# Performance work log

Measured on AMD Instinct MI355X. Metric: run time of the kernel, lower is better.

## Reference

```python
import jax, jax.numpy as jnp
import numpy as np

V, D, H, L = 50000, 50, 50, 100   # vocab, input_dim, hidden_dim, latent_dim
WIN = 5
B = 65536
MARGIN = 1.0


def setup_inputs() -> dict:
    key = jax.random.key(0)
    ks = jax.random.split(key, 12)
    emb = jax.random.normal(ks[0], (V, D), jnp.float32) * 0.1
    emb = emb.at[0].set(0.0)  # padding_idx=0
    W1 = jax.random.normal(ks[1], (2 * D, H), jnp.float32) * 0.1
    b1 = jnp.zeros((H,), jnp.float32)
    Wmu = jax.random.normal(ks[2], (H, L), jnp.float32) * 0.1
    bmu = jnp.zeros((L,), jnp.float32)
    Wls = jax.random.normal(ks[3], (H, 1), jnp.float32) * 0.1
    bls = jnp.zeros((1,), jnp.float32)
    type_means_tbl = jax.random.normal(ks[4], (V, L), jnp.float32) * 0.1
    type_logvars_tbl = jax.random.normal(ks[5], (V, 1), jnp.float32) * 0.1
    centers = jax.random.randint(ks[6], (B,), 1, V, jnp.int32)
    contexts = jax.random.randint(ks[7], (B, 2 * WIN), 1, V, jnp.int32)
    neg_contexts = jax.random.randint(ks[8], (B, 2 * WIN), 1, V, jnp.int32)
    return {"emb": emb, "W1": W1, "b1": b1, "Wmu": Wmu, "bmu": bmu,
            "Wls": Wls, "bls": bls, "type_means_tbl": type_means_tbl,
            "type_logvars_tbl": type_logvars_tbl, "centers": centers,
            "contexts": contexts, "neg_contexts": neg_contexts}


def _kl(idx, post_mu, post_logsigma, type_means_tbl, type_logvars_tbl):
    # idx: [N] int; post_mu: [N,L]; post_logsigma: [N,1]
    post_sigma = jnp.exp(post_logsigma)                      # [N,1]
    type_mean = type_means_tbl[idx]                          # [N,L]
    type_logvar = type_logvars_tbl[idx]                      # [N,1]
    type_var = jnp.exp(type_logvar)                          # [N,1]
    var_division = post_sigma / type_var                     # [N,1]
    diff = post_mu - type_mean                               # [N,L]
    diff_term = jnp.sum(diff * diff, axis=1, keepdims=True) / type_var  # [N,1]
    logvar_division = type_logvar - post_logsigma            # [N,1]
    return 0.5 * ((var_division + diff_term + logvar_division)[:, 0] - L)  # [N]


def reference(emb, W1, b1, Wmu, bmu, Wls, bls, type_means_tbl, type_logvars_tbl,
              centers, contexts, neg_contexts):
    Bn, C = contexts.shape                                   # C = 2*window
    e_ctx = emb[contexts]                                    # [B,C,D]
    e_cen = emb[centers]                                     # [B,D]
    # concat(context_embed, center_repeat) along feature dim -> [B,C,2D]
    cat = jnp.concatenate(
        [e_ctx, jnp.broadcast_to(e_cen[:, None, :], (Bn, C, D))], axis=-1)
    h = jax.nn.relu(jnp.einsum('bcf,fh->bch', cat, W1) + b1).sum(axis=1)  # [B,H]
    mu = h @ Wmu + bmu                                       # [B,L]
    logsigma = h @ Wls + bls                                 # [B,1]
    # repeat each row 2*window times (matches repeat(1,2w).view(-1,L))
    mus = jnp.repeat(mu, C, axis=0)                          # [B*C,L]
    logsigmas = jnp.repeat(logsigma, C, axis=0)              # [B*C,1]
    kl_ctx = _kl(contexts.reshape(-1), mus, logsigmas, type_means_tbl, type_logvars_tbl)
    kl_neg = _kl(neg_contexts.reshape(-1), mus, logsigmas, type_means_tbl, type_logvars_tbl)
    kl_cen = _kl(centers, mu, logsigma, type_means_tbl, type_logvars_tbl)
    hinge = jnp.maximum(kl_ctx - kl_neg + MARGIN, 0.0)
    loss = hinge.sum() + kl_cen.sum()
    return loss / Bn
```

## Files before the change

kernel.cpp:

```cpp
#include <hip/hip_runtime.h>

namespace {
constexpr int V    = 50000;
constexpr int D    = 50;
constexpr int H    = 50;
constexpr int LDIM = 100;
constexpr int C    = 10;
constexpr int B    = 65536;
constexpr int NTILES = B / 16;

constexpr size_t OFF_EMB  = 0;
constexpr size_t OFF_TM   = OFF_EMB + (size_t)V * 64 * 2;
constexpr size_t OFF_W1T  = OFF_TM + (size_t)V * 128;
constexpr size_t OFF_W1B  = OFF_W1T + 2 * 4 * 64 * 8 * 2;
constexpr size_t OFF_WMU  = OFF_W1B + 2 * 4 * 64 * 8 * 2;
constexpr size_t OFF_B1P  = OFF_WMU + 2 * 7 * 64 * 8 * 2;
constexpr size_t OFF_BMUP = OFF_B1P + 64 * 4;
constexpr size_t OFF_WLSP = OFF_BMUP + 128 * 4;
constexpr size_t OFF_TT   = OFF_WLSP + 64 * 4;
constexpr size_t OFF_MUF  = OFF_TT + (size_t)V * 16;
constexpr size_t OFF_MSL  = OFF_MUF + (size_t)NTILES * 4 * 64 * 8;
constexpr size_t OFF_PART = OFF_MSL + (size_t)B * 16;
constexpr size_t WS_NEED  = OFF_PART + (size_t)NTILES * 4;

typedef __attribute__((ext_vector_type(8))) short short8;
typedef __attribute__((ext_vector_type(4))) float f32x4;
typedef unsigned long long ull;

__device__ __forceinline__ unsigned short f2bf(float x) {
  unsigned u = __builtin_bit_cast(unsigned, x);
  unsigned r = (u + 0x7FFFu + ((u >> 16) & 1u)) >> 16;
  return (unsigned short)r;
}

__global__ __launch_bounds__(256) void bsg_prep(
    const float* __restrict__ emb, const float* __restrict__ tm,
    const float* __restrict__ tlv, const float* __restrict__ W1,
    const float* __restrict__ Wmu, const float* __restrict__ b1,
    const float* __restrict__ bmu, const float* __restrict__ Wls,
    unsigned short* __restrict__ embB, unsigned char* __restrict__ tmF8,
    float4* __restrict__ tt4, unsigned short* __restrict__ w1t,
    unsigned short* __restrict__ w1b, unsigned short* __restrict__ wmuB,
    float* __restrict__ b1p, float* __restrict__ bmup, float* __restrict__ wlsp) {
  const int EMB_T = V * 8;
  const int TM_T  = V * 8;
  const int stride = gridDim.x * blockDim.x;
  for (int t = blockIdx.x * blockDim.x + threadIdx.x; t < EMB_T + TM_T; t += stride) {
    if (t < EMB_T) {
      int v = t >> 3, c = t & 7, k0 = c * 8;
      unsigned short r[8];
#pragma unroll
      for (int e = 0; e < 8; ++e) {
        int k = k0 + e;
        r[e] = f2bf(k < D ? emb[(size_t)v * D + k] : 0.f);
      }
      uint4 o;
      o.x = (unsigned)r[0] | ((unsigned)r[1] << 16);
      o.y = (unsigned)r[2] | ((unsigned)r[3] << 16);
      o.z = (unsigned)r[4] | ((unsigned)r[5] << 16);
      o.w = (unsigned)r[6] | ((unsigned)r[7] << 16);
      ((uint4*)(embB + (size_t)v * 64))[c] = o;
    } else {
      int t2 = t - EMB_T;
      int v = t2 >> 3, c = t2 & 7, k0 = c * 16;
      float val[16];
#pragma unroll
      for (int e = 0; e < 16; ++e) {
        int k = k0 + e;
        val[e] = (k < LDIM) ? tm[(size_t)v * LDIM + k] : 0.f;
      }
      uint4 o;
      unsigned dw[4];
      float sq = 0.f;
#pragma unroll
      for (int j = 0; j < 4; ++j) {
        int d = __builtin_amdgcn_cvt_pk_fp8_f32(val[4 * j + 0], val[4 * j + 1], 0, false);
        d = __builtin_amdgcn_cvt_pk_fp8_f32(val[4 * j + 2], val[4 * j + 3], d, true);
        dw[j] = (unsigned)d;
        float q0 = __builtin_amdgcn_cvt_f32_fp8(d, 0);
        float q1 = __builtin_amdgcn_cvt_f32_fp8(d, 1);
        float q2 = __builtin_amdgcn_cvt_f32_fp8(d, 2);
        float q3 = __builtin_amdgcn_cvt_f32_fp8(d, 3);
        sq = fmaf(q0, q0, sq); sq = fmaf(q1, q1, sq);
        sq = fmaf(q2, q2, sq); sq = fmaf(q3, q3, sq);
      }
      o.x = dw[0]; o.y = dw[1]; o.z = dw[2]; o.w = dw[3];
      ((uint4*)(tmF8 + (size_t)v * 128))[c] = o;
#pragma unroll
      for (int off = 1; off < 8; off <<= 1) sq += __shfl_xor(sq, off);
      if (c == 0) {
        float tl = tlv[v];
        float4 q;
        q.x = tl; q.y = __expf(-tl); q.z = sq; q.w = 0.f;
        tt4[v] = q;
      }
    }
  }
  if (blockIdx.x == 0) {
    const int tid = threadIdx.x;
    for (int id = tid; id < 1024; id += 256) {
      int half = id >> 9, rem = id & 511;
      int ks = rem >> 8, nt = (rem >> 6) & 3, l = rem & 63;
      unsigned short r[8];
      int n = nt * 16 + (l & 15);
#pragma unroll
      for (int e = 0; e < 8; ++e) {
        int f = ks * 32 + ((l >> 4) << 3) + e;
        float v = (f < D && n < H) ? W1[(size_t)(half * D + f) * H + n] : 0.f;
        r[e] = f2bf(v);
      }
      uint4 o;
      o.x = (unsigned)r[0] | ((unsigned)r[1] << 16);
      o.y = (unsigned)r[2] | ((unsigned)r[3] << 16);
      o.z = (unsigned)r[4] | ((unsigned)r[5] << 16);
      o.w = (unsigned)r[6] | ((unsigned)r[7] << 16);
      unsigned short* dst = half ? w1b : w1t;
      ((uint4*)dst)[(ks * 4 + nt) * 64 + l] = o;
    }
    for (int id = tid; id < 896; id += 256) {
      int ks = id / 448, rem = id % 448;
      int nt = rem >> 6, l = rem & 63;
      unsigned short r[8];
      int n = nt * 16 + (l & 15);
#pragma unroll
      for (int e = 0; e < 8; ++e) {
        int j = ks * 32 + ((l >> 4) << 3) + e;
        float v = (j < H && n < LDIM) ? Wmu[(size_t)j * LDIM + n] : 0.f;
        r[e] = f2bf(v);
      }
      uint4 o;
      o.x = (unsigned)r[0] | ((unsigned)r[1] << 16);
      o.y = (unsigned)r[2] | ((unsigned)r[3] << 16);
      o.z = (unsigned)r[4] | ((unsigned)r[5] << 16);
      o.w = (unsigned)r[6] | ((unsigned)r[7] << 16);
      ((uint4*)wmuB)[(ks * 7 + nt) * 64 + l] = o;
    }
    if (tid < 64)  b1p[tid]  = (tid < H)    ? b1[tid]  : 0.f;
    if (tid < 128) bmup[tid] = (tid < LDIM) ? bmu[tid] : 0.f;
    if (tid < 64)  wlsp[tid] = (tid < H)    ? Wls[tid] : 0.f;
  }
}

__global__ __launch_bounds__(256, 3) void bsg_mlp(
    const unsigned short* __restrict__ embB,
    const unsigned short* __restrict__ w1t,
    const unsigned short* __restrict__ w1b,
    const unsigned short* __restrict__ wmuB,
    const float* __restrict__ b1p, const float* __restrict__ bmup,
    const float* __restrict__ wlsp, const float* __restrict__ bls,
    const int* __restrict__ centers, const int* __restrict__ contexts,
    ull* __restrict__ muF, float4* __restrict__ msl) {
  __shared__ unsigned short hlds[32][64];
  __shared__ unsigned char kb[2][16][128];
  __shared__ float logsp[2][32];
  __shared__ float musq_p[2][2][16];
  __shared__ char stg[4][4 * 2048];

  const int tid = threadIdx.x;
  const int w = tid >> 6, l = tid & 63;
  const int srow = l & 15, kc = l >> 4;
  const int st = w & 1, np = w >> 1;
  const int sblk = blockIdx.x * 32;
  const int sg = sblk + st * 16 + srow;
  const int s3 = srow & 3;

  char* kbbase = (char*)&kb[0][0][0];
  auto kb_ptr = [&](int st_, int s_, int kbyte) -> char* {
    return kbbase + st_ * 2048 + s_ * 128 + (kbyte ^ ((s_ & 7) << 4));
  };

  {
    int st_ = tid >> 7, rem = tid & 127;
    int s_ = rem >> 3, j = rem & 7;
    *(unsigned short*)kb_ptr(st_, s_, 112 + 2 * j) = 0;
  }

  char* myl = &stg[w][0];
  const int cofs = ((kc ^ s3) << 4);
  const int aoff = ((kc ^ s3) << 8) + (srow << 4);

  int rid[11];
  rid[0] = centers[sg];
#pragma unroll
  for (int c = 0; c < 10; ++c) rid[1 + c] = contexts[sg * 10 + c];

  const short8* w1tF = (const short8*)w1t;
  const short8* w1bF = (const short8*)w1b;

  short8 Bz[2][2], Bt[2][2];
#pragma unroll
  for (int n2 = 0; n2 < 2; ++n2)
#pragma unroll
    for (int ks = 0; ks < 2; ++ks) {
      Bz[n2][ks] = w1bF[(ks * 4 + 2 * np + n2) * 64 + l];
      Bt[n2][ks] = w1tF[(ks * 4 + 2 * np + n2) * 64 + l];
    }
  float b1v[2] = {b1p[(2 * np + 0) * 16 + srow], b1p[(2 * np + 1) * 16 + srow]};

  const unsigned char* embBy = (const unsigned char*)embB;

  f32x4 Z0 = {0.f, 0.f, 0.f, 0.f}, Z1 = {0.f, 0.f, 0.f, 0.f};
  f32x4 hv0 = {0.f, 0.f, 0.f, 0.f}, hv1 = {0.f, 0.f, 0.f, 0.f};

#define MLP_STAGE(T)                                                         \
  do {                                                                       \
    const unsigned char* src_ = embBy + (size_t)rid[(T)] * 128 + cofs;       \
    char* d0_ = myl + ((T) & 3) * 2048;                                      \
    __builtin_amdgcn_global_load_lds(                                        \
        (const __attribute__((address_space(1))) unsigned int*)src_,         \
        (__attribute__((address_space(3))) unsigned int*)d0_, 16, 0, 0);     \
    __builtin_amdgcn_global_load_lds(                                        \
        (const __attribute__((address_space(1))) unsigned int*)(src_ + 64),  \
        (__attribute__((address_space(3))) unsigned int*)(d0_ + 1024),       \
        16, 0, 0);                                                           \
  } while (0)

#define MLP_STEP(T, NW)                                                      \
  do {                                                                       \
    if ((T) + 3 < 11) MLP_STAGE((T) + 3);                                    \
    asm volatile("s_waitcnt vmcnt(" #NW ")" ::: "memory");                   \
    __builtin_amdgcn_sched_barrier(0);                                       \
    const char* sb_ = myl + ((T) & 3) * 2048;                                \
    short8 A0_ = *(const short8*)(sb_ + aoff);                               \
    short8 A1_ = *(const short8*)(sb_ + 1024 + aoff);                        \
    if ((T) == 0) {                                                          \
      Z0 = __builtin_amdgcn_mfma_f32_16x16x32_bf16(A0_, Bz[0][0], Z0, 0, 0, 0); \
      Z0 = __builtin_amdgcn_mfma_f32_16x16x32_bf16(A1_, Bz[0][1], Z0, 0, 0, 0); \
      Z1 = __builtin_amdgcn_mfma_f32_16x16x32_bf16(A0_, Bz[1][0], Z1, 0, 0, 0); \
      Z1 = __builtin_amdgcn_mfma_f32_16x16x32_bf16(A1_, Bz[1][1], Z1, 0, 0, 0); \
    } else {                                                                 \
      f32x4 ac0_ = {0.f, 0.f, 0.f, 0.f}, ac1_ = {0.f, 0.f, 0.f, 0.f};        \
      ac0_ = __builtin_amdgcn_mfma_f32_16x16x32_bf16(A0_, Bt[0][0], ac0_, 0, 0, 0); \
      ac0_ = __builtin_amdgcn_mfma_f32_16x16x32_bf16(A1_, Bt[0][1], ac0_, 0, 0, 0); \
      ac1_ = __builtin_amdgcn_mfma_f32_16x16x32_bf16(A0_, Bt[1][0], ac1_, 0, 0, 0); \
      ac1_ = __builtin_amdgcn_mfma_f32_16x16x32_bf16(A1_, Bt[1][1], ac1_, 0, 0, 0); \
      _Pragma("unroll")                                                      \
      for (int q = 0; q < 4; ++q) {                                          \
        hv0[q] += fmaxf(ac0_[q] + Z0[q] + b1v[0], 0.f);                      \
        hv1[q] += fmaxf(ac1_[q] + Z1[q] + b1v[1], 0.f);                      \
      }                                                                      \
    }                                                                        \
  } while (0)

  MLP_STAGE(0);
  MLP_STAGE(1);
  MLP_STAGE(2);

  MLP_STEP(0, 6); MLP_STEP(1, 6); MLP_STEP(2, 6); MLP_STEP(3, 6);
  MLP_STEP(4, 6); MLP_STEP(5, 6); MLP_STEP(6, 6); MLP_STEP(7, 6);
  MLP_STEP(8, 4); MLP_STEP(9, 2); MLP_STEP(10, 0);

#undef MLP_STEP
#undef MLP_STAGE

  {
    float wl0 = wlsp[(2 * np + 0) * 16 + srow];
    float wl1 = wlsp[(2 * np + 1) * 16 + srow];
    float lp[4];
#pragma unroll
    for (int q = 0; q < 4; ++q) lp[q] = hv0[q] * wl0 + hv1[q] * wl1;
#pragma unroll
    for (int off = 1; off < 16; off <<= 1)
#pragma unroll
      for (int q = 0; q < 4; ++q) lp[q] += __shfl_xor(lp[q], off);
    if (srow == 0) {
#pragma unroll
      for (int q = 0; q < 4; ++q) logsp[np][st * 16 + kc * 4 + q] = lp[q];
    }
  }
#pragma unroll
  for (int q = 0; q < 4; ++q) {
    hlds[st * 16 + kc * 4 + q][(2 * np + 0) * 16 + srow] = f2bf(hv0[q]);
    hlds[st * 16 + kc * 4 + q][(2 * np + 1) * 16 + srow] = f2bf(hv1[q]);
  }
  __syncthreads();

  {
    const short8* hrow = (const short8*)&hlds[st * 16 + srow][0];
    short8 Ah0 = hrow[kc], Ah1 = hrow[4 + kc];
    const short8* wmF = (const short8*)wmuB;
    f32x4 sqv = {0.f, 0.f, 0.f, 0.f};
    for (int nt = np; nt < 7; nt += 2) {
      short8 B0 = wmF[(0 * 7 + nt) * 64 + l];
      short8 B1 = wmF[(1 * 7 + nt) * 64 + l];
      f32x4 m = {0.f, 0.f, 0.f, 0.f};
      m = __builtin_amdgcn_mfma_f32_16x16x32_bf16(Ah0, B0, m, 0, 0, 0);
      m = __builtin_amdgcn_mfma_f32_16x16x32_bf16(Ah1, B1, m, 0, 0, 0);
      int lcol = nt * 16 + srow;
      float bm = bmup[lcol];
      float mv0 = m[0] + bm, mv1 = m[1] + bm, mv2 = m[2] + bm, mv3 = m[3] + bm;
      int d01 = __builtin_amdgcn_cvt_pk_fp8_f32(mv0, mv1, 0, false);
      int d23 = __builtin_amdgcn_cvt_pk_fp8_f32(mv2, mv3, 0, false);
      float q0 = __builtin_amdgcn_cvt_f32_fp8(d01, 0);
      float q1 = __builtin_amdgcn_cvt_f32_fp8(d01, 1);
      float q2 = __builtin_amdgcn_cvt_f32_fp8(d23, 0);
      float q3 = __builtin_amdgcn_cvt_f32_fp8(d23, 1);
      sqv[0] = fmaf(q0, q0, sqv[0]);
      sqv[1] = fmaf(q1, q1, sqv[1]);
      sqv[2] = fmaf(q2, q2, sqv[2]);
      sqv[3] = fmaf(q3, q3, sqv[3]);
      *(unsigned char*)kb_ptr(st, kc * 4 + 0, lcol) = (unsigned char)(d01 & 0xFF);
      *(unsigned char*)kb_ptr(st, kc * 4 + 1, lcol) = (unsigned char)((d01 >> 8) & 0xFF);
      *(unsigned char*)kb_ptr(st, kc * 4 + 2, lcol) = (unsigned char)(d23 & 0xFF);
      *(unsigned char*)kb_ptr(st, kc * 4 + 3, lcol) = (unsigned char)((d23 >> 8) & 0xFF);
    }
#pragma unroll
    for (int off = 1; off < 16; off <<= 1)
#pragma unroll
      for (int q = 0; q < 4; ++q) sqv[q] += __shfl_xor(sqv[q], off);
    if (srow == 0) {
#pragma unroll
      for (int q = 0; q < 4; ++q) musq_p[np][st][kc * 4 + q] = sqv[q];
    }
  }
  __syncthreads();

  if (w < 2) {
    size_t gt = (size_t)blockIdx.x * 2 + w;
#pragma unroll
    for (int ks = 0; ks < 4; ++ks) {
      ull v = *(const ull*)kb_ptr(w, srow, ks * 32 + kc * 8);
      muF[(gt * 4 + ks) * 64 + l] = v;
    }
  } else if (w == 2 && l < 32) {
    int s_ = l;
    float lg = bls[0] + logsp[0][s_] + logsp[1][s_];
    float msq = musq_p[0][s_ >> 4][s_ & 15] + musq_p[1][s_ >> 4][s_ & 15];
    float4 o;
    o.x = lg; o.y = __expf(lg); o.z = msq; o.w = 0.f;
    msl[sblk + s_] = o;
  }
}

__global__ __launch_bounds__(256) void bsg_kl(
    const unsigned char* __restrict__ tmF8, const float4* __restrict__ tt4,
    const ull* __restrict__ muF, const float4* __restrict__ msl,
    const int* __restrict__ centers, const int* __restrict__ contexts,
    const int* __restrict__ negctx, float* __restrict__ partials) {
  __shared__ char klds[4][4 * 2048];

  const int w = threadIdx.x >> 6, l = threadIdx.x & 63;
  const int gt = blockIdx.x * 4 + w;
  const int srow = l & 15, kc = l >> 4;
  const int s = gt * 16 + srow;
  const int s3 = srow & 3;

  char* myl = &klds[w][0];
  const int cofs = ((kc ^ s3) << 4);
  const int rA = ((((kc >> 1) ^ s3) * 16 + srow) * 16) + (kc & 1) * 8;
  const int rB = ((((2 + (kc >> 1)) ^ s3) * 16 + srow) * 16) + (kc & 1) * 8;

  ull Bmu[4];
#pragma unroll
  for (int ks = 0; ks < 4; ++ks) Bmu[ks] = muF[((size_t)gt * 4 + ks) * 64 + l];

  const float4 m = msl[s];
  const float lg = m.x, ps = m.y, msq = m.z;
  const bool isdiag = (kc == (srow >> 2));
  const int qd = srow & 3;

  int idx[21];
  idx[0] = centers[s];
#pragma unroll
  for (int c = 0; c < 10; ++c) idx[1 + c] = contexts[s * 10 + c];
#pragma unroll
  for (int c = 0; c < 10; ++c) idx[11 + c] = negctx[s * 10 + c];

  constexpr int ord[21] = {0, 1, 11, 2, 12, 3, 13, 4, 14, 5, 15,
                           6, 16, 7, 17, 8, 18, 9, 19, 10, 20};

  float4 ttb[4];
  float loss = 0.f, klc = 0.f;

#define KL_STAGE(T)                                                          \
  do {                                                                       \
    const unsigned char* src_ = tmF8 + (size_t)idx[ord[(T)]] * 128 + cofs;   \
    char* d0_ = myl + ((T) & 3) * 2048;                                      \
    __builtin_amdgcn_global_load_lds(                                        \
        (const __attribute__((address_space(1))) unsigned int*)src_,         \
        (__attribute__((address_space(3))) unsigned int*)d0_, 16, 0, 0);     \
    __builtin_amdgcn_global_load_lds(                                        \
        (const __attribute__((address_space(1))) unsigned int*)(src_ + 64),  \
        (__attribute__((address_space(3))) unsigned int*)(d0_ + 1024),       \
        16, 0, 0);                                                           \
    ttb[(T) & 3] = tt4[idx[ord[(T)]]];                                       \
  } while (0)

#define KL_STEP(T, NW)                                                       \
  do {                                                                       \
    if ((T) + 3 < 21) KL_STAGE((T) + 3);                                     \
    asm volatile("s_waitcnt vmcnt(" #NW ")" ::: "memory");                   \
    __builtin_amdgcn_sched_barrier(0);                                       \
    const char* kb_ = myl + ((T) & 3) * 2048;                                \
    ull a0_ = *(const ull*)(kb_ + rA);                                       \
    ull a1_ = *(const ull*)(kb_ + rB);                                       \
    ull a2_ = *(const ull*)(kb_ + rA + 1024);                                \
    ull a3_ = *(const ull*)(kb_ + rB + 1024);                                \
    f32x4 acc_ = {0.f, 0.f, 0.f, 0.f};                                       \
    acc_ = __builtin_amdgcn_mfma_f32_16x16x32_fp8_fp8((long)a0_, (long)Bmu[0], acc_, 0, 0, 0); \
    acc_ = __builtin_amdgcn_mfma_f32_16x16x32_fp8_fp8((long)a1_, (long)Bmu[1], acc_, 0, 0, 0); \
    acc_ = __builtin_amdgcn_mfma_f32_16x16x32_fp8_fp8((long)a2_, (long)Bmu[2], acc_, 0, 0, 0); \
    acc_ = __builtin_amdgcn_mfma_f32_16x16x32_fp8_fp8((long)a3_, (long)Bmu[3], acc_, 0, 0, 0); \
    float4 tv_ = ttb[(T) & 3];                                               \
    float dot_ = (qd & 2) ? ((qd & 1) ? acc_[3] : acc_[2])                   \
                          : ((qd & 1) ? acc_[1] : acc_[0]);                  \
    float dsum_ = msq + tv_.z - 2.f * dot_;                                  \
    float kl_ = 0.5f * (fmaf(ps + dsum_, tv_.y, tv_.x - lg) - (float)LDIM);  \
    if ((T) == 0)      loss += isdiag ? kl_ : 0.f;                           \
    else if ((T) & 1)  klc = kl_;                                            \
    else               loss += isdiag ? fmaxf(klc - kl_ + 1.f, 0.f) : 0.f;   \
  } while (0)

  KL_STAGE(0);
  KL_STAGE(1);
  KL_STAGE(2);

  KL_STEP(0, 6);  KL_STEP(1, 6);  KL_STEP(2, 6);  KL_STEP(3, 6);
  KL_STEP(4, 6);  KL_STEP(5, 6);  KL_STEP(6, 6);  KL_STEP(7, 6);
  KL_STEP(8, 6);  KL_STEP(9, 6);  KL_STEP(10, 6); KL_STEP(11, 6);
  KL_STEP(12, 6); KL_STEP(13, 6); KL_STEP(14, 6); KL_STEP(15, 6);
  KL_STEP(16, 6); KL_STEP(17, 6); KL_STEP(18, 4); KL_STEP(19, 2);
  KL_STEP(20, 0);

#undef KL_STEP
#undef KL_STAGE

#pragma unroll
  for (int off = 32; off > 0; off >>= 1) loss += __shfl_down(loss, off);
  if (l == 0) partials[gt] = loss;
}

__global__ __launch_bounds__(256) void bsg_reduce(const float* __restrict__ partials,
                                                  int n, float* __restrict__ out) {
  double v = 0.0;
  for (int i = threadIdx.x; i < n; i += 256) v += (double)partials[i];
#pragma unroll
  for (int off = 32; off > 0; off >>= 1) v += __shfl_down(v, off);
  __shared__ double ws4[4];
  if ((threadIdx.x & 63) == 0) ws4[threadIdx.x >> 6] = v;
  __syncthreads();
  if (threadIdx.x == 0) {
    double t = 0.0;
#pragma unroll
    for (int k = 0; k < 4; ++k) t += ws4[k];
    out[0] = (float)(t / (double)B);
  }
}

__device__ __forceinline__ float kl_term_fb(const float* mu, float ps, float logs,
                                            int idx, const float* tm_tbl,
                                            const float* tlv_tbl) {
  const float* tm = tm_tbl + (size_t)idx * LDIM;
  float tlv = tlv_tbl[idx];
  float d0 = 0.f, d1 = 0.f, d2 = 0.f, d3 = 0.f;
#pragma unroll
  for (int l = 0; l < LDIM; l += 4) {
    float4 t = *reinterpret_cast<const float4*>(tm + l);
    float a0 = mu[l] - t.x, a1 = mu[l + 1] - t.y;
    float a2 = mu[l + 2] - t.z, a3 = mu[l + 3] - t.w;
    d0 = fmaf(a0, a0, d0); d1 = fmaf(a1, a1, d1);
    d2 = fmaf(a2, a2, d2); d3 = fmaf(a3, a3, d3);
  }
  return 0.5f * (fmaf(ps + (d0 + d1) + (d2 + d3), __expf(-tlv), tlv - logs) - (float)LDIM);
}

__global__ __launch_bounds__(256) void bsg_fb(
    const float* __restrict__ emb, const float* __restrict__ W1,
    const float* __restrict__ b1, const float* __restrict__ Wmu,
    const float* __restrict__ bmu, const float* __restrict__ Wls,
    const float* __restrict__ bls, const float* __restrict__ tm_tbl,
    const float* __restrict__ tlv_tbl, const int* __restrict__ centers,
    const int* __restrict__ contexts, const int* __restrict__ negctx,
    float* __restrict__ partials) {
  const int b = blockIdx.x * 256 + threadIdx.x;
  const int cen = centers[b];
  float ecen[D];
  const float* ep = emb + (size_t)cen * D;
#pragma unroll
  for (int f = 0; f < D; f += 2) {
    float2 v = *reinterpret_cast<const float2*>(ep + f);
    ecen[f] = v.x; ecen[f + 1] = v.y;
  }
  float z[H];
#pragma unroll
  for (int j = 0; j < H; ++j) z[j] = b1[j];
#pragma unroll
  for (int f = 0; f < D; ++f) {
    float vf = ecen[f];
#pragma unroll
    for (int j = 0; j < H; ++j) z[j] = fmaf(vf, W1[(D + f) * H + j], z[j]);
  }
  float h[H];
#pragma unroll
  for (int j = 0; j < H; ++j) h[j] = 0.f;
  for (int c = 0; c < C; ++c) {
    const float* ecp = emb + (size_t)contexts[b * C + c] * D;
    float s[H];
#pragma unroll
    for (int j = 0; j < H; ++j) s[j] = z[j];
#pragma unroll
    for (int f = 0; f < D; ++f) {
      float vf = ecp[f];
#pragma unroll
      for (int j = 0; j < H; ++j) s[j] = fmaf(vf, W1[f * H + j], s[j]);
    }
#pragma unroll
    for (int j = 0; j < H; ++j) h[j] += fmaxf(s[j], 0.f);
  }
  float mu[LDIM];
#pragma unroll
  for (int l = 0; l < LDIM; ++l) mu[l] = bmu[l];
#pragma unroll
  for (int j = 0; j < H; ++j) {
    float hj = h[j];
#pragma unroll
    for (int l = 0; l < LDIM; ++l) mu[l] = fmaf(hj, Wmu[j * LDIM + l], mu[l]);
  }
  float logs = bls[0];
#pragma unroll
  for (int j = 0; j < H; ++j) logs = fmaf(h[j], Wls[j], logs);
  float ps = __expf(logs);
  float acc = kl_term_fb(mu, ps, logs, cen, tm_tbl, tlv_tbl);
  for (int c = 0; c < C; ++c) {
    float kc = kl_term_fb(mu, ps, logs, contexts[b * C + c], tm_tbl, tlv_tbl);
    float kn = kl_term_fb(mu, ps, logs, negctx[b * C + c], tm_tbl, tlv_tbl);
    acc += fmaxf(kc - kn + 1.f, 0.f);
  }
  float vs = acc;
#pragma unroll
  for (int off = 32; off > 0; off >>= 1) vs += __shfl_down(vs, off);
  __shared__ float wsum[4];
  if ((threadIdx.x & 63) == 0) wsum[threadIdx.x >> 6] = vs;
  __syncthreads();
  if (threadIdx.x == 0) {
    float t = 0.f;
#pragma unroll
    for (int k = 0; k < 4; ++k) t += wsum[k];
    partials[blockIdx.x] = t;
  }
}
}

extern "C" void kernel_launch(void* const* d_in, const int* in_sizes, int n_in,
                              void* d_out, int out_size, void* d_ws, size_t ws_size,
                              hipStream_t stream) {
  const float* emb     = (const float*)d_in[0];
  const float* W1      = (const float*)d_in[1];
  const float* b1      = (const float*)d_in[2];
  const float* Wmu     = (const float*)d_in[3];
  const float* bmu     = (const float*)d_in[4];
  const float* Wls     = (const float*)d_in[5];
  const float* bls     = (const float*)d_in[6];
  const float* tm      = (const float*)d_in[7];
  const float* tlv     = (const float*)d_in[8];
  const int*   centers = (const int*)d_in[9];
  const int*   ctx     = (const int*)d_in[10];
  const int*   negc    = (const int*)d_in[11];
  float* out = (float*)d_out;

  if (ws_size < WS_NEED + 1024) {
    float* partials = (float*)d_ws;
    bsg_fb<<<256, 256, 0, stream>>>(emb, W1, b1, Wmu, bmu, Wls, bls, tm, tlv,
                                    centers, ctx, negc, partials);
    bsg_reduce<<<1, 256, 0, stream>>>(partials, 256, out);
    return;
  }

  char* ws = (char*)d_ws;
  unsigned short* embB = (unsigned short*)(ws + OFF_EMB);
  unsigned char*  tmF8 = (unsigned char*)(ws + OFF_TM);
  unsigned short* w1t  = (unsigned short*)(ws + OFF_W1T);
  unsigned short* w1b  = (unsigned short*)(ws + OFF_W1B);
  unsigned short* wmuB = (unsigned short*)(ws + OFF_WMU);
  float* b1p  = (float*)(ws + OFF_B1P);
  float* bmup = (float*)(ws + OFF_BMUP);
  float* wlsp = (float*)(ws + OFF_WLSP);
  float4* tt4 = (float4*)(ws + OFF_TT);
  ull* muF    = (ull*)(ws + OFF_MUF);
  float4* msl = (float4*)(ws + OFF_MSL);
  float* partials = (float*)(ws + OFF_PART);

  bsg_prep<<<1024, 256, 0, stream>>>(emb, tm, tlv, W1, Wmu, b1, bmu, Wls,
                                     embB, tmF8, tt4, w1t, w1b, wmuB, b1p, bmup, wlsp);
  bsg_mlp<<<B / 32, 256, 0, stream>>>(embB, w1t, w1b, wmuB, b1p, bmup, wlsp, bls,
                                      centers, ctx, muF, msl);
  bsg_kl<<<NTILES / 4, 256, 0, stream>>>(tmF8, tt4, muF, msl, centers, ctx, negc,
                                         partials);
  bsg_reduce<<<1, 256, 0, stream>>>(partials, NTILES, out);
}
```

Baseline: 76.27 us.

## Fuse MLP and KL kernels, splitting context pairs across waves

Result: no change. 76.43 us (+0.2%).

```diff
diff --git a/kernel.cpp b/kernel.cpp
--- a/kernel.cpp
+++ b/kernel.cpp
@@ -7,7 +7,7 @@
 constexpr int LDIM = 100;
 constexpr int C    = 10;
 constexpr int B    = 65536;
-constexpr int NTILES = B / 16;
+constexpr int NPART = (B / 32) * 4;
 
 constexpr size_t OFF_EMB  = 0;
 constexpr size_t OFF_TM   = OFF_EMB + (size_t)V * 64 * 2;
@@ -18,10 +18,8 @@
 constexpr size_t OFF_BMUP = OFF_B1P + 64 * 4;
 constexpr size_t OFF_WLSP = OFF_BMUP + 128 * 4;
 constexpr size_t OFF_TT   = OFF_WLSP + 64 * 4;
-constexpr size_t OFF_MUF  = OFF_TT + (size_t)V * 16;
-constexpr size_t OFF_MSL  = OFF_MUF + (size_t)NTILES * 4 * 64 * 8;
-constexpr size_t OFF_PART = OFF_MSL + (size_t)B * 16;
-constexpr size_t WS_NEED  = OFF_PART + (size_t)NTILES * 4;
+constexpr size_t OFF_PART = OFF_TT + (size_t)V * 16;
+constexpr size_t WS_NEED  = OFF_PART + (size_t)NPART * 4;
 
 typedef __attribute__((ext_vector_type(8))) short short8;
 typedef __attribute__((ext_vector_type(4))) float f32x4;
@@ -141,15 +139,16 @@
   }
 }
 
-__global__ __launch_bounds__(256, 3) void bsg_mlp(
+__global__ __launch_bounds__(256, 3) void bsg_main(
     const unsigned short* __restrict__ embB,
+    const unsigned char* __restrict__ tmF8, const float4* __restrict__ tt4,
     const unsigned short* __restrict__ w1t,
     const unsigned short* __restrict__ w1b,
     const unsigned short* __restrict__ wmuB,
     const float* __restrict__ b1p, const float* __restrict__ bmup,
     const float* __restrict__ wlsp, const float* __restrict__ bls,
     const int* __restrict__ centers, const int* __restrict__ contexts,
-    ull* __restrict__ muF, float4* __restrict__ msl) {
+    const int* __restrict__ negctx, float* __restrict__ partials) {
   __shared__ unsigned short hlds[32][64];
   __shared__ unsigned char kb[2][16][128];
   __shared__ float logsp[2][32];
@@ -178,6 +177,8 @@
   char* myl = &stg[w][0];
   const int cofs = ((kc ^ s3) << 4);
   const int aoff = ((kc ^ s3) << 8) + (srow << 4);
+  const int rA = ((((kc >> 1) ^ s3) * 16 + srow) * 16) + (kc & 1) * 8;
+  const int rB = ((((2 + (kc >> 1)) ^ s3) * 16 + srow) * 16) + (kc & 1) * 8;
 
   int rid[11];
   rid[0] = centers[sg];
@@ -315,66 +316,33 @@
   }
   __syncthreads();
 
-  if (w < 2) {
-    size_t gt = (size_t)blockIdx.x * 2 + w;
-#pragma unroll
-    for (int ks = 0; ks < 4; ++ks) {
-      ull v = *(const ull*)kb_ptr(w, srow, ks * 32 + kc * 8);
-      muF[(gt * 4 + ks) * 64 + l] = v;
-    }
-  } else if (w == 2 && l < 32) {
-    int s_ = l;
-    float lg = bls[0] + logsp[0][s_] + logsp[1][s_];
-    float msq = musq_p[0][s_ >> 4][s_ & 15] + musq_p[1][s_ >> 4][s_ & 15];
-    float4 o;
-    o.x = lg; o.y = __expf(lg); o.z = msq; o.w = 0.f;
-    msl[sblk + s_] = o;
-  }
-}
-
-__global__ __launch_bounds__(256) void bsg_kl(
-    const unsigned char* __restrict__ tmF8, const float4* __restrict__ tt4,
-    const ull* __restrict__ muF, const float4* __restrict__ msl,
-    const int* __restrict__ centers, const int* __restrict__ contexts,
-    const int* __restrict__ negctx, float* __restrict__ partials) {
-  __shared__ char klds[4][4 * 2048];
-
-  const int w = threadIdx.x >> 6, l = threadIdx.x & 63;
-  const int gt = blockIdx.x * 4 + w;
-  const int srow = l & 15, kc = l >> 4;
-  const int s = gt * 16 + srow;
-  const int s3 = srow & 3;
-
-  char* myl = &klds[w][0];
-  const int cofs = ((kc ^ s3) << 4);
-  const int rA = ((((kc >> 1) ^ s3) * 16 + srow) * 16) + (kc & 1) * 8;
-  const int rB = ((((2 + (kc >> 1)) ^ s3) * 16 + srow) * 16) + (kc & 1) * 8;
-
-  ull Bmu[4];
-#pragma unroll
-  for (int ks = 0; ks < 4; ++ks) Bmu[ks] = muF[((size_t)gt * 4 + ks) * 64 + l];
-
-  const float4 m = msl[s];
-  const float lg = m.x, ps = m.y, msq = m.z;
+  const int p = np;
+  const float lg = bls[0] + logsp[0][st * 16 + srow] + logsp[1][st * 16 + srow];
+  const float ps = __expf(lg);
+  const float msq = musq_p[0][st][srow] + musq_p[1][st][srow];
   const bool isdiag = (kc == (srow >> 2));
   const int qd = srow & 3;
 
-  int idx[21];
-  idx[0] = centers[s];
-#pragma unroll
-  for (int c = 0; c < 10; ++c) idx[1 + c] = contexts[s * 10 + c];
-#pragma unroll
-  for (int c = 0; c < 10; ++c) idx[11 + c] = negctx[s * 10 + c];
-
-  constexpr int ord[21] = {0, 1, 11, 2, 12, 3, 13, 4, 14, 5, 15,
-                           6, 16, 7, 17, 8, 18, 9, 19, 10, 20};
+  ull Bmu[4];
+#pragma unroll
+  for (int ks = 0; ks < 4; ++ks)
+    Bmu[ks] = *(const ull*)kb_ptr(st, srow, ks * 32 + kc * 8);
+
+  int kidx[11];
+  kidx[0] = rid[0];
+#pragma unroll
+  for (int i = 0; i < 5; ++i) {
+    int c = p + 2 * i;
+    kidx[1 + 2 * i] = rid[1 + c];
+    kidx[2 + 2 * i] = negctx[sg * 10 + c];
+  }
 
   float4 ttb[4];
   float loss = 0.f, klc = 0.f;
 
 #define KL_STAGE(T)                                                          \
   do {                                                                       \
-    const unsigned char* src_ = tmF8 + (size_t)idx[ord[(T)]] * 128 + cofs;   \
+    const unsigned char* src_ = tmF8 + (size_t)kidx[(T)] * 128 + cofs;       \
     char* d0_ = myl + ((T) & 3) * 2048;                                      \
     __builtin_amdgcn_global_load_lds(                                        \
         (const __attribute__((address_space(1))) unsigned int*)src_,         \
@@ -383,12 +351,12 @@
         (const __attribute__((address_space(1))) unsigned int*)(src_ + 64),  \
         (__attribute__((address_space(3))) unsigned int*)(d0_ + 1024),       \
         16, 0, 0);                                                           \
-    ttb[(T) & 3] = tt4[idx[ord[(T)]]];                                       \
+    ttb[(T) & 3] = tt4[kidx[(T)]];                                           \
   } while (0)
 
 #define KL_STEP(T, NW)                                                       \
   do {                                                                       \
-    if ((T) + 3 < 21) KL_STAGE((T) + 3);                                     \
+    if ((T) + 3 < 11) KL_STAGE((T) + 3);                                     \
     asm volatile("s_waitcnt vmcnt(" #NW ")" ::: "memory");                   \
     __builtin_amdgcn_sched_barrier(0);                                       \
     const char* kb_ = myl + ((T) & 3) * 2048;                                \
@@ -406,7 +374,7 @@
                           : ((qd & 1) ? acc_[1] : acc_[0]);                  \
     float dsum_ = msq + tv_.z - 2.f * dot_;                                  \
     float kl_ = 0.5f * (fmaf(ps + dsum_, tv_.y, tv_.x - lg) - (float)LDIM);  \
-    if ((T) == 0)      loss += isdiag ? kl_ : 0.f;                           \
+    if ((T) == 0)      loss += (isdiag && p == 0) ? kl_ : 0.f;               \
     else if ((T) & 1)  klc = kl_;                                            \
     else               loss += isdiag ? fmaxf(klc - kl_ + 1.f, 0.f) : 0.f;   \
   } while (0)
@@ -415,19 +383,16 @@
   KL_STAGE(1);
   KL_STAGE(2);
 
-  KL_STEP(0, 6);  KL_STEP(1, 6);  KL_STEP(2, 6);  KL_STEP(3, 6);
-  KL_STEP(4, 6);  KL_STEP(5, 6);  KL_STEP(6, 6);  KL_STEP(7, 6);
-  KL_STEP(8, 6);  KL_STEP(9, 6);  KL_STEP(10, 6); KL_STEP(11, 6);
-  KL_STEP(12, 6); KL_STEP(13, 6); KL_STEP(14, 6); KL_STEP(15, 6);
-  KL_STEP(16, 6); KL_STEP(17, 6); KL_STEP(18, 4); KL_STEP(19, 2);
-  KL_STEP(20, 0);
+  KL_STEP(0, 6); KL_STEP(1, 6); KL_STEP(2, 6); KL_STEP(3, 6);
+  KL_STEP(4, 6); KL_STEP(5, 6); KL_STEP(6, 6); KL_STEP(7, 6);
+  KL_STEP(8, 4); KL_STEP(9, 2); KL_STEP(10, 0);
 
 #undef KL_STEP
 #undef KL_STAGE
 
 #pragma unroll
   for (int off = 32; off > 0; off >>= 1) loss += __shfl_down(loss, off);
-  if (l == 0) partials[gt] = loss;
+  if (l == 0) partials[blockIdx.x * 4 + w] = loss;
 }
 
 __global__ __launch_bounds__(256) void bsg_reduce(const float* __restrict__ partials,
@@ -576,15 +541,12 @@
   float* bmup = (float*)(ws + OFF_BMUP);
   float* wlsp = (float*)(ws + OFF_WLSP);
   float4* tt4 = (float4*)(ws + OFF_TT);
-  ull* muF    = (ull*)(ws + OFF_MUF);
-  float4* msl = (float4*)(ws + OFF_MSL);
   float* partials = (float*)(ws + OFF_PART);
 
   bsg_prep<<<1024, 256, 0, stream>>>(emb, tm, tlv, W1, Wmu, b1, bmu, Wls,
                                      embB, tmF8, tt4, w1t, w1b, wmuB, b1p, bmup, wlsp);
-  bsg_mlp<<<B / 32, 256, 0, stream>>>(embB, w1t, w1b, wmuB, b1p, bmup, wlsp, bls,
-                                      centers, ctx, muF, msl);
-  bsg_kl<<<NTILES / 4, 256, 0, stream>>>(tmF8, tt4, muF, msl, centers, ctx, negc,
-                                         partials);
-  bsg_reduce<<<1, 256, 0, stream>>>(partials, NTILES, out);
-}
+  bsg_main<<<B / 32, 256, 0, stream>>>(embB, tmF8, tt4, w1t, w1b, wmuB,
+                                       b1p, bmup, wlsp, bls, centers, ctx, negc,
+                                       partials);
+  bsg_reduce<<<1, 256, 0, stream>>>(partials, NPART, out);
+}
```
